# Optimization experiments

Hardware: AMD Instinct MI355X
Metric: run time of the kernel (lower is better)

## Reference

```python
import jax, jax.numpy as jnp
import numpy as np

N = 50000      # nodes
E = 500000     # edges
D = 128        # in_dim == out_dim
L = 4          # encoder_layers
G = 64         # graphs in batch
FIXED = 10000  # fixed_input_dim
BN_EPS = 1e-5


def setup_inputs() -> dict:
    key = jax.random.key(0)
    ks = jax.random.split(key, 14)
    s = 0.05
    feat_id = jax.random.randint(ks[0], (N,), 0, FIXED)
    edge_index = jax.random.randint(ks[1], (2, E), 0, N)
    # sorted graph assignment guaranteeing all G graphs are non-empty
    batch = (jnp.arange(N) * G) // N
    return {
        "feat_id": feat_id,
        "edge_index": edge_index,
        "batch": batch,
        # value_projection: Linear(FIXED, D); store weight.T as a lookup table
        "value_proj_w": jax.random.normal(ks[2], (FIXED, D)) * s,
        "value_proj_b": jax.random.normal(ks[3], (D,)) * s,
        "deg_emb": jax.random.normal(ks[4], (1001, D)) * s,
        # stacked per-layer GIN MLP params: Linear -> BN -> ReLU -> Linear
        "mlp_w1": jax.random.normal(ks[5], (L, D, D)) * s,
        "mlp_b1": jax.random.normal(ks[6], (L, D)) * s,
        "bn1_g": 1.0 + 0.1 * jax.random.normal(ks[7], (L, D)),
        "bn1_b": 0.1 * jax.random.normal(ks[8], (L, D)),
        "mlp_w2": jax.random.normal(ks[9], (L, D, D)) * s,
        "mlp_b2": jax.random.normal(ks[10], (L, D)) * s,
        # outer per-layer BatchNorm1d
        "bn2_g": 1.0 + 0.1 * jax.random.normal(ks[11], (L, D)),
        "bn2_b": 0.1 * jax.random.normal(ks[12], (L, D)),
    }


def _bn(x, g, b):
    # BatchNorm1d in training mode: batch stats over the node axis, biased var
    mu = jnp.mean(x, axis=0)
    var = jnp.mean(jnp.square(x - mu), axis=0)
    return g * (x - mu) * jax.lax.rsqrt(var + BN_EPS) + b


def reference(feat_id, edge_index, batch, value_proj_w, value_proj_b, deg_emb,
              mlp_w1, mlp_b1, bn1_g, bn1_b, mlp_w2, mlp_b2, bn2_g, bn2_b):
    src, dst = edge_index[0], edge_index[1]
    # one_hot(feat_id % FIXED) @ W.T + b  ==  gather of transposed weight rows
    h_attr = value_proj_w[feat_id % FIXED] + value_proj_b  # [N, D]
    # in-degree embedding (clamped to [0, 1000])
    in_deg = jax.ops.segment_sum(jnp.ones((E,), jnp.int32), dst, num_segments=N)
    h = h_attr + deg_emb[jnp.clip(in_deg, 0, 1000)]
    for i in range(L):
        # GIN: sum_{j in N(v)} h_j + (1 + eps) * h_v, eps = 0 (learn_eps=False)
        agg = jax.ops.segment_sum(h[src], dst, num_segments=N) + h
        z = jax.nn.relu(_bn(agg @ mlp_w1[i] + mlp_b1[i], bn1_g[i], bn1_b[i]))
        z = z @ mlp_w2[i] + mlp_b2[i]
        h = jax.nn.relu(_bn(z, bn2_g[i], bn2_b[i]))
    # global mean pool per graph
    gsum = jax.ops.segment_sum(h, batch, num_segments=G)       # [G, D]
    cnt = jax.ops.segment_sum(jnp.ones((N, 1)), batch, num_segments=G)
    graph_feature = gsum / jnp.maximum(cnt, 1.0)
    return graph_feature, h
```

## Files before the change

### kernel.cpp

```cpp
#include <hip/hip_runtime.h>

#define NN 50000
#define NE 500000
#define DD 128
#define NL 4
#define NG 64
#define FIXED_DIM 10000
#define BN_EPS 1e-5f
#define NB 196

typedef unsigned short u16;
typedef unsigned int u32;
typedef __attribute__((ext_vector_type(8))) short bf16x8;
typedef __attribute__((ext_vector_type(4))) float f32x4;

__device__ __forceinline__ float bf2f(u16 u) {
    return __uint_as_float(((u32)u) << 16);
}
__device__ __forceinline__ u16 f2bf(float f) {
    u32 u = __float_as_uint(f);
    return (u16)((u + 0x7FFFu + ((u >> 16) & 1u)) >> 16);
}
__device__ __forceinline__ float ldf(const void* p, size_t i, int isbf) {
    return isbf ? bf2f(((const u16*)p)[i]) : ((const float*)p)[i];
}

__global__ void k_pre(const void* __restrict__ vb, int* __restrict__ flag,
                      const int* __restrict__ batch, int* __restrict__ goff,
                      float* __restrict__ zbase, int zwords) {
    int b = blockIdx.x, t = threadIdx.x;
    if (b == 0) {
        __shared__ int ok[256];
        float v = (t < 128) ? bf2f(((const u16*)vb)[t]) : 0.f;
        ok[t] = (t < 128) ? ((fabsf(v) < 1000.f) ? 1 : 0) : 1;
        __syncthreads();
        for (int off = 128; off; off >>= 1) {
            if (t < off) ok[t] &= ok[t + off];
            __syncthreads();
        }
        if (t == 0) *flag = ok[0];
    } else if (b == 1) {
        if (t <= NG) {
            int lo = 0, hi = NN;
            while (lo < hi) {
                int mid = (lo + hi) >> 1;
                if (batch[mid] < t) lo = mid + 1; else hi = mid;
            }
            goff[t] = lo;
        }
    } else {
        int i = (b - 2) * 256 + t;
        if (i < zwords) zbase[i] = 0.f;
    }
}

__global__ void k_cvtswz(const void* b1, const void* b2, const void* g1,
                         const void* be1, const void* g2, const void* be2,
                         const void* __restrict__ w1, const void* __restrict__ w2,
                         float* __restrict__ pc, u16* __restrict__ Wsw,
                         const int* __restrict__ flag) {
    int b = blockIdx.x, tt = threadIdx.x;
    if (b < 12) {
        int t = b * 256 + tt;
        int p = t >> 9, j = t & 511;
        const void* s = (p == 0) ? b1 : (p == 1) ? b2 : (p == 2) ? g1
                      : (p == 3) ? be1 : (p == 4) ? g2 : be2;
        pc[t] = ldf(s, j, *flag);
    } else {
        int t = (b - 12) * 256 + tt;
        int m    = t >> 14;
        int idx  = t & 16383;
        int nt   = idx >> 11;
        int ks   = (idx >> 9) & 3;
        int lane = (idx >> 3) & 63;
        int j    = idx & 7;
        int row = ks * 32 + (lane >> 4) * 8 + j;
        int col = nt * 16 + (lane & 15);
        const void* src = (m < 4) ? w1 : w2;
        size_t off = (size_t)(m & 3) * DD * DD + (size_t)row * DD + col;
        Wsw[t] = f2bf(ldf(src, off, *flag));
    }
}

__global__ void k_deg(const int* __restrict__ dst, int* __restrict__ deg) {
    int i = blockIdx.x * 256 + threadIdx.x;
    if (i < NE) atomicAdd(&deg[dst[i]], 1);
}

__global__ void k_scan12(const int* __restrict__ deg, int* __restrict__ bsum,
                         int* __restrict__ sem) {
    __shared__ int S[256];
    __shared__ int lastB;
    int b = blockIdx.x, t = threadIdx.x;
    int i = b * 256 + t;
    S[t] = (i < NN) ? deg[i] : 0;
    __syncthreads();
    for (int off = 128; off; off >>= 1) {
        if (t < off) S[t] += S[t + off];
        __syncthreads();
    }
    if (t == 0) {
        atomicExch(&bsum[b], S[0]);
        __threadfence();
        lastB = (atomicAdd(&sem[0], 1) == gridDim.x - 1);
    }
    __syncthreads();
    if (!lastB) return;
    __threadfence();
    int v = (t < NB) ? atomicAdd(&bsum[t], 0) : 0;
    S[t] = v;
    __syncthreads();
    for (int off = 1; off < 256; off <<= 1) {
        int x = (t >= off) ? S[t - off] : 0;
        __syncthreads();
        S[t] += x;
        __syncthreads();
    }
    if (t < NB) bsum[t] = S[t] - v;
}

__global__ void k_scan3init(const int* __restrict__ deg, const int* __restrict__ bsum,
                            int* __restrict__ rowptr,
                            const int* __restrict__ feat, const void* __restrict__ vw,
                            const void* __restrict__ vb, const void* __restrict__ demb,
                            u16* __restrict__ B, const int* __restrict__ flag) {
    __shared__ int S[256];
    int b = blockIdx.x, t = threadIdx.x;
    if (b < NB) {
        int i = b * 256 + t;
        int v = (i < NN) ? deg[i] : 0;
        S[t] = v;
        __syncthreads();
        for (int off = 1; off < 256; off <<= 1) {
            int x = (t >= off) ? S[t - off] : 0;
            __syncthreads();
            S[t] += x;
            __syncthreads();
        }
        if (i < NN) rowptr[i] = bsum[b] + S[t] - v;
        if (i == NN - 1) rowptr[NN] = bsum[b] + S[t];
    } else {
        int idx = (b - NB) * 256 + t;
        if (idx >= NN * DD) return;
        int n = idx >> 7, c = idx & 127;
        int isbf = *flag;
        int f = feat[n] % FIXED_DIM;
        int dg = min(deg[n], 1000);
        B[idx] = f2bf(ldf(vw, (size_t)f * DD + c, isbf)
                    + ldf(vb, c, isbf)
                    + ldf(demb, (size_t)dg * DD + c, isbf));
    }
}

__global__ void k_fill(const int* __restrict__ src, const int* __restrict__ dst,
                       const int* __restrict__ rowptr, int* __restrict__ cursor,
                       int* __restrict__ colidx) {
    int e = blockIdx.x * 256 + threadIdx.x;
    if (e >= NE) return;
    int d = dst[e];
    int p = atomicAdd(&cursor[d], 1);
    colidx[rowptr[d] + p] = src[e];
}

template <bool AFF>
__global__ __launch_bounds__(256, 8) void k_aggr(
        const u16* __restrict__ B, const int* __restrict__ rowptr,
        const int* __restrict__ colidx,
        const float* __restrict__ gIn, const float* __restrict__ bIn,
        const float* __restrict__ sIn, const float* __restrict__ qIn,
        u16* __restrict__ Agg) {
    int n = blockIdx.x * 4 + (threadIdx.x >> 6);
    if (n >= NN) return;
    int c = (threadIdx.x & 63) * 2;
    float a0 = 1.f, b0 = 0.f, a1 = 1.f, b1 = 0.f;
    if (AFF) {
        float inv = 1.0f / (float)NN;
        float mu0 = sIn[c] * inv, mu1 = sIn[c + 1] * inv;
        float v0 = fmaxf(qIn[c] * inv - mu0 * mu0, 0.f);
        float v1 = fmaxf(qIn[c + 1] * inv - mu1 * mu1, 0.f);
        a0 = gIn[c] * rsqrtf(v0 + BN_EPS);
        a1 = gIn[c + 1] * rsqrtf(v1 + BN_EPS);
        b0 = bIn[c] - a0 * mu0;
        b1 = bIn[c + 1] - a1 * mu1;
    }
    u32 w = *(const u32*)&B[(size_t)n * DD + c];
    float x0 = bf2f((u16)(w & 0xFFFF)), x1 = bf2f((u16)(w >> 16));
    float s0 = AFF ? fmaxf(fmaf(a0, x0, b0), 0.f) : x0;
    float s1 = AFF ? fmaxf(fmaf(a1, x1, b1), 0.f) : x1;
    int lo = rowptr[n], hi = rowptr[n + 1];
    int j = lo;
    for (; j + 4 <= hi; j += 4) {
        int m0 = colidx[j], m1 = colidx[j + 1];
        int m2 = colidx[j + 2], m3 = colidx[j + 3];
        u32 w0 = *(const u32*)&B[(size_t)m0 * DD + c];
        u32 w1v = *(const u32*)&B[(size_t)m1 * DD + c];
        u32 w2v = *(const u32*)&B[(size_t)m2 * DD + c];
        u32 w3v = *(const u32*)&B[(size_t)m3 * DD + c];
        float y;
        y = bf2f((u16)(w0 & 0xFFFF)); s0 += AFF ? fmaxf(fmaf(a0, y, b0), 0.f) : y;
        y = bf2f((u16)(w0 >> 16));    s1 += AFF ? fmaxf(fmaf(a1, y, b1), 0.f) : y;
        y = bf2f((u16)(w1v & 0xFFFF)); s0 += AFF ? fmaxf(fmaf(a0, y, b0), 0.f) : y;
        y = bf2f((u16)(w1v >> 16));    s1 += AFF ? fmaxf(fmaf(a1, y, b1), 0.f) : y;
        y = bf2f((u16)(w2v & 0xFFFF)); s0 += AFF ? fmaxf(fmaf(a0, y, b0), 0.f) : y;
        y = bf2f((u16)(w2v >> 16));    s1 += AFF ? fmaxf(fmaf(a1, y, b1), 0.f) : y;
        y = bf2f((u16)(w3v & 0xFFFF)); s0 += AFF ? fmaxf(fmaf(a0, y, b0), 0.f) : y;
        y = bf2f((u16)(w3v >> 16));    s1 += AFF ? fmaxf(fmaf(a1, y, b1), 0.f) : y;
    }
    for (; j < hi; j++) {
        int m = colidx[j];
        w = *(const u32*)&B[(size_t)m * DD + c];
        x0 = bf2f((u16)(w & 0xFFFF)); x1 = bf2f((u16)(w >> 16));
        s0 += AFF ? fmaxf(fmaf(a0, x0, b0), 0.f) : x0;
        s1 += AFF ? fmaxf(fmaf(a1, x1, b1), 0.f) : x1;
    }
    *(u32*)&Agg[(size_t)n * DD + c] = ((u32)f2bf(s1) << 16) | (u32)f2bf(s0);
}

template <bool IN16, bool OUT16, bool AFF>
__global__ __launch_bounds__(256, 3) void k_gemm(
        const void* In, const u16* __restrict__ Wsw,
        const float* __restrict__ bias,
        const float* __restrict__ gIn, const float* __restrict__ bIn,
        const float* __restrict__ sIn, const float* __restrict__ qIn,
        void* Out, float* __restrict__ ssum, float* __restrict__ ssq,
        int nRows) {
    __shared__ u16 Wl[16384];
    __shared__ u16 At[64 * 136];
    __shared__ float affS[256];
    float* RedS = (float*)At;
    float* RedQ = RedS + 512;
    const int t = threadIdx.x;
    const int row0 = blockIdx.x * 64;

    if (AFF) {
        if (t < 128) {
            float inv = 1.0f / (float)NN;
            float mu = sIn[t] * inv;
            float var = fmaxf(qIn[t] * inv - mu * mu, 0.f);
            float a = gIn[t] * rsqrtf(var + BN_EPS);
            affS[t] = a;
            affS[128 + t] = bIn[t] - a * mu;
        }
        __syncthreads();
    }

    {
        const uint4* s = (const uint4*)Wsw;
        uint4* d = (uint4*)Wl;
        #pragma unroll
        for (int i = 0; i < 8; i++) d[t + i * 256] = s[t + i * 256];
    }
    if (IN16) {
        #pragma unroll
        for (int i = t; i < 1024; i += 256) {
            int r  = i >> 4;
            int c8 = (i & 15) * 8;
            int gr = row0 + r;
            uint4 v = make_uint4(0u, 0u, 0u, 0u);
            if (gr < nRows) v = *(const uint4*)&((const u16*)In)[(size_t)gr * DD + c8];
            *(uint4*)&At[r * 136 + c8] = v;
        }
    } else {
        #pragma unroll
        for (int i = t; i < 2048; i += 256) {
            int r  = i >> 5;
            int c4 = (i & 31) * 4;
            int gr = row0 + r;
            float4 v = make_float4(0.f, 0.f, 0.f, 0.f);
            if (gr < nRows) {
                v = *(const float4*)&((const float*)In)[(size_t)gr * DD + c4];
                if (AFF) {
                    v.x = fmaxf(fmaf(affS[c4 + 0], v.x, affS[128 + c4 + 0]), 0.f);
                    v.y = fmaxf(fmaf(affS[c4 + 1], v.y, affS[128 + c4 + 1]), 0.f);
                    v.z = fmaxf(fmaf(affS[c4 + 2], v.z, affS[128 + c4 + 2]), 0.f);
                    v.w = fmaxf(fmaf(affS[c4 + 3], v.w, affS[128 + c4 + 3]), 0.f);
                }
            }
            ushort4 o;
            o.x = f2bf(v.x); o.y = f2bf(v.y); o.z = f2bf(v.z); o.w = f2bf(v.w);
            *(ushort4*)&At[r * 136 + c4] = o;
        }
    }
    __syncthreads();

    const int w    = t >> 6;
    const int ln   = t & 63;
    const int quad = ln >> 4;
    const int lq   = ln & 15;

    f32x4 acc[8];
    #pragma unroll
    for (int nt = 0; nt < 8; nt++) acc[nt] = (f32x4){0.f, 0.f, 0.f, 0.f};

    const u16* aRow = &At[(w * 16 + lq) * 136 + quad * 8];
    #pragma unroll
    for (int ks = 0; ks < 4; ks++) {
        bf16x8 a = *(const bf16x8*)&aRow[ks * 32];
        #pragma unroll
        for (int nt = 0; nt < 8; nt++) {
            bf16x8 b = *(const bf16x8*)&Wl[((nt * 4 + ks) * 64 + ln) * 8];
            acc[nt] = __builtin_amdgcn_mfma_f32_16x16x32_bf16(a, b, acc[nt], 0, 0, 0);
        }
    }
    __syncthreads();

    const int rb = row0 + w * 16 + quad * 4;
    #pragma unroll
    for (int nt = 0; nt < 8; nt++) {
        int col = nt * 16 + lq;
        float bv = bias[col];
        float s = 0.f, q = 0.f;
        #pragma unroll
        for (int r = 0; r < 4; r++) {
            int gr = rb + r;
            if (gr < nRows) {
                float val = acc[nt][r] + bv;
                size_t o = (size_t)gr * DD + col;
                if (OUT16) ((u16*)Out)[o] = f2bf(val);
                else       ((float*)Out)[o] = val;
                s += val; q += val * val;
            }
        }
        s += __shfl_xor(s, 16); q += __shfl_xor(q, 16);
        s += __shfl_xor(s, 32); q += __shfl_xor(q, 32);
        if (quad == 0) { RedS[w * 128 + col] = s; RedQ[w * 128 + col] = q; }
    }
    __syncthreads();
    if (t < 128) {
        float s = RedS[t] + RedS[128 + t] + RedS[256 + t] + RedS[384 + t];
        float q = RedQ[t] + RedQ[128 + t] + RedQ[256 + t] + RedQ[384 + t];
        atomicAdd(&ssum[t], s);
        atomicAdd(&ssq[t], q);
    }
}

__global__ __launch_bounds__(256, 4) void k_upool(
        const u16* __restrict__ Bz,
        const float* __restrict__ gIn, const float* __restrict__ bIn,
        const float* __restrict__ sIn, const float* __restrict__ qIn,
        const int* __restrict__ batch, float* __restrict__ A,
        float* __restrict__ gsum, const int* __restrict__ goff,
        float* __restrict__ outw, int* __restrict__ sem) {
    const int t = threadIdx.x;
    const int c = t & 127;
    const int half = t >> 7;
    const int r0 = blockIdx.x * 64;
    float inv = 1.0f / (float)NN;
    float mu = sIn[c] * inv;
    float var = fmaxf(qIn[c] * inv - mu * mu, 0.f);
    float a = gIn[c] * rsqrtf(var + BN_EPS);
    float bb = bIn[c] - a * mu;
    float acc = 0.f;
    int curg = -1;
    for (int i = 0; i < 32; i++) {
        int r = r0 + half + 2 * i;
        if (r >= NN) break;
        int gg = batch[r];
        if (gg != curg) {
            if (curg >= 0) atomicAdd(&gsum[(size_t)curg * DD + c], acc);
            acc = 0.f; curg = gg;
        }
        float v = fmaxf(fmaf(a, bf2f(Bz[(size_t)r * DD + c]), bb), 0.f);
        A[(size_t)r * DD + c] = v;
        acc += v;
    }
    if (curg >= 0) atomicAdd(&gsum[(size_t)curg * DD + c], acc);

    __shared__ int lastF;
    if (t == 0) {
        __threadfence();
        lastF = (atomicAdd(&sem[1], 1) == gridDim.x - 1);
    }
    __syncthreads();
    if (!lastF) return;
    __threadfence();
    for (int i = t; i < NG * DD; i += 256) {
        int g = i >> 7;
        float cnt = fmaxf((float)(goff[g + 1] - goff[g]), 1.0f);
        outw[i] = atomicAdd(&gsum[i], 0.0f) / cnt;
    }
}

extern "C" void kernel_launch(void* const* d_in, const int* in_sizes, int n_in,
                              void* d_out, int out_size, void* d_ws, size_t ws_size,
                              hipStream_t stream) {
    const int* feat  = (const int*)d_in[0];
    const int* ei    = (const int*)d_in[1];
    const int* batch = (const int*)d_in[2];
    const void* vw   = d_in[3];
    const void* vb   = d_in[4];
    const void* demb = d_in[5];
    const void* w1   = d_in[6];
    const void* b1   = d_in[7];
    const void* g1   = d_in[8];
    const void* be1  = d_in[9];
    const void* w2   = d_in[10];
    const void* b2   = d_in[11];
    const void* g2   = d_in[12];
    const void* be2  = d_in[13];

    const int* src = ei;
    const int* dst = ei + NE;
    const size_t ND = (size_t)NN * DD;

    float* pc     = (float*)d_ws;
    int*   flag   = (int*)(pc + 3072);
    float* stats  = (float*)(flag + 64);
    float* gsum   = stats + 2048;
    int*   deg    = (int*)(gsum + 8192);
    int*   cursor = deg + NN;
    int*   sem    = cursor + NN;
    int*   bsum   = sem + 64;
    int*   goff   = bsum + 256;
    int*   rowptr = goff + 128;
    int*   colidx = rowptr + NN + 64;
    u16*   Wsw    = (u16*)(colidx + NE);
    u16*   B      = Wsw + 8 * 16384;
    u16*   Agg16  = B + ND;

    float* b1c  = pc;
    float* b2c  = pc + 512;
    float* g1c  = pc + 1024;
    float* be1c = pc + 1536;
    float* g2c  = pc + 2048;
    float* be2c = pc + 2560;
    float* sum1 = stats;
    float* sq1  = stats + 512;
    float* sum2 = stats + 1024;
    float* sq2  = stats + 1536;

    float* outw = (float*)d_out;
    float* A    = outw + (size_t)NG * DD;

    const int zwords = 2048 + 8192 + NN + NN + 64;
    const int gridND = (int)(ND / 256);
    const int gemmBlocks = (NN + 63) / 64;
    const int aggrBlocks = (NN + 3) / 4;

    k_pre<<<2 + (zwords + 255) / 256, 256, 0, stream>>>(vb, flag, batch, goff,
                                                        stats, zwords);
    k_cvtswz<<<12 + 512, 256, 0, stream>>>(b1, b2, g1, be1, g2, be2, w1, w2,
                                           pc, Wsw, flag);
    k_deg<<<(NE + 255) / 256, 256, 0, stream>>>(dst, deg);
    k_scan12<<<NB, 256, 0, stream>>>(deg, bsum, sem);
    k_scan3init<<<NB + gridND, 256, 0, stream>>>(deg, bsum, rowptr,
                                                 feat, vw, vb, demb, B, flag);
    k_fill<<<(NE + 255) / 256, 256, 0, stream>>>(src, dst, rowptr, cursor, colidx);

    for (int l = 0; l < NL; l++) {
        const u16* W1l = Wsw + (size_t)l * 16384;
        const u16* W2l = Wsw + (size_t)(4 + l) * 16384;
        if (l == 0) {
            k_aggr<false><<<aggrBlocks, 256, 0, stream>>>(
                B, rowptr, colidx, nullptr, nullptr, nullptr, nullptr, Agg16);
        } else {
            k_aggr<true><<<aggrBlocks, 256, 0, stream>>>(
                B, rowptr, colidx, g2c + (l - 1) * 128, be2c + (l - 1) * 128,
                sum2 + (l - 1) * 128, sq2 + (l - 1) * 128, Agg16);
        }
        k_gemm<true, false, false><<<gemmBlocks, 256, 0, stream>>>(
            Agg16, W1l, b1c + l * 128, nullptr, nullptr, nullptr, nullptr,
            A, sum1 + l * 128, sq1 + l * 128, NN);
        k_gemm<false, true, true><<<gemmBlocks, 256, 0, stream>>>(
            A, W2l, b2c + l * 128, g1c + l * 128, be1c + l * 128,
            sum1 + l * 128, sq1 + l * 128,
            B, sum2 + l * 128, sq2 + l * 128, NN);
    }
    k_upool<<<(NN + 63) / 64, 256, 0, stream>>>(
        B, g2c + 3 * 128, be2c + 3 * 128, sum2 + 3 * 128, sq2 + 3 * 128,
        batch, A, gsum, goff, outw, sem);
}
```

Measured before the change: 643.5 us.

## Double GEMM row tile to 128 and vectorize pooling kernel column access

The GEMM kernel now processes 128 rows per block, with each wave computing two 16-row MFMA tiles that share the same B fragments. This amortizes the per-block copy of the 32KB weight matrix into LDS across twice as many rows and halves the LDS reads of B per output. Occupancy drops to two blocks per CU because of the larger LDS and register footprint. Separately, the unpool/mean-pool kernel now has each thread handle two adjacent columns with 32-bit loads and float2 stores.

```diff
diff --git a/kernel.cpp b/kernel.cpp
--- a/kernel.cpp
+++ b/kernel.cpp
@@ -217,7 +217,7 @@
 }
 
 template <bool IN16, bool OUT16, bool AFF>
-__global__ __launch_bounds__(256, 3) void k_gemm(
+__global__ __launch_bounds__(256, 2) void k_gemm(
         const void* In, const u16* __restrict__ Wsw,
         const float* __restrict__ bias,
         const float* __restrict__ gIn, const float* __restrict__ bIn,
@@ -225,12 +225,12 @@
         void* Out, float* __restrict__ ssum, float* __restrict__ ssq,
         int nRows) {
     __shared__ u16 Wl[16384];
-    __shared__ u16 At[64 * 136];
+    __shared__ u16 At[128 * 136];
     __shared__ float affS[256];
     float* RedS = (float*)At;
     float* RedQ = RedS + 512;
     const int t = threadIdx.x;
-    const int row0 = blockIdx.x * 64;
+    const int row0 = blockIdx.x * 128;
 
     if (AFF) {
         if (t < 128) {
@@ -251,8 +251,7 @@
         for (int i = 0; i < 8; i++) d[t + i * 256] = s[t + i * 256];
     }
     if (IN16) {
-        #pragma unroll
-        for (int i = t; i < 1024; i += 256) {
+        for (int i = t; i < 2048; i += 256) {
             int r  = i >> 4;
             int c8 = (i & 15) * 8;
             int gr = row0 + r;
@@ -261,8 +260,7 @@
             *(uint4*)&At[r * 136 + c8] = v;
         }
     } else {
-        #pragma unroll
-        for (int i = t; i < 2048; i += 256) {
+        for (int i = t; i < 4096; i += 256) {
             int r  = i >> 5;
             int c4 = (i & 31) * 4;
             int gr = row0 + r;
@@ -288,23 +286,30 @@
     const int quad = ln >> 4;
     const int lq   = ln & 15;
 
-    f32x4 acc[8];
+    f32x4 acc0[8], acc1[8];
     #pragma unroll
-    for (int nt = 0; nt < 8; nt++) acc[nt] = (f32x4){0.f, 0.f, 0.f, 0.f};
-
-    const u16* aRow = &At[(w * 16 + lq) * 136 + quad * 8];
+    for (int nt = 0; nt < 8; nt++) {
+        acc0[nt] = (f32x4){0.f, 0.f, 0.f, 0.f};
+        acc1[nt] = (f32x4){0.f, 0.f, 0.f, 0.f};
+    }
+
+    const u16* aRow0 = &At[(w * 32 + lq) * 136 + quad * 8];
+    const u16* aRow1 = &At[(w * 32 + 16 + lq) * 136 + quad * 8];
     #pragma unroll
     for (int ks = 0; ks < 4; ks++) {
-        bf16x8 a = *(const bf16x8*)&aRow[ks * 32];
+        bf16x8 a0 = *(const bf16x8*)&aRow0[ks * 32];
+        bf16x8 a1 = *(const bf16x8*)&aRow1[ks * 32];
         #pragma unroll
         for (int nt = 0; nt < 8; nt++) {
             bf16x8 b = *(const bf16x8*)&Wl[((nt * 4 + ks) * 64 + ln) * 8];
-            acc[nt] = __builtin_amdgcn_mfma_f32_16x16x32_bf16(a, b, acc[nt], 0, 0, 0);
-        }
-    }
-    __syncthreads();
-
-    const int rb = row0 + w * 16 + quad * 4;
+            acc0[nt] = __builtin_amdgcn_mfma_f32_16x16x32_bf16(a0, b, acc0[nt], 0, 0, 0);
+            acc1[nt] = __builtin_amdgcn_mfma_f32_16x16x32_bf16(a1, b, acc1[nt], 0, 0, 0);
+        }
+    }
+    __syncthreads();
+
+    const int rb0 = row0 + w * 32 + quad * 4;
+    const int rb1 = rb0 + 16;
     #pragma unroll
     for (int nt = 0; nt < 8; nt++) {
         int col = nt * 16 + lq;
@@ -312,9 +317,20 @@
         float s = 0.f, q = 0.f;
         #pragma unroll
         for (int r = 0; r < 4; r++) {
-            int gr = rb + r;
+            int gr = rb0 + r;
             if (gr < nRows) {
-                float val = acc[nt][r] + bv;
+                float val = acc0[nt][r] + bv;
+                size_t o = (size_t)gr * DD + col;
+                if (OUT16) ((u16*)Out)[o] = f2bf(val);
+                else       ((float*)Out)[o] = val;
+                s += val; q += val * val;
+            }
+        }
+        #pragma unroll
+        for (int r = 0; r < 4; r++) {
+            int gr = rb1 + r;
+            if (gr < nRows) {
+                float val = acc1[nt][r] + bv;
                 size_t o = (size_t)gr * DD + col;
                 if (OUT16) ((u16*)Out)[o] = f2bf(val);
                 else       ((float*)Out)[o] = val;
@@ -342,29 +358,40 @@
         float* __restrict__ gsum, const int* __restrict__ goff,
         float* __restrict__ outw, int* __restrict__ sem) {
     const int t = threadIdx.x;
-    const int c = t & 127;
-    const int half = t >> 7;
+    const int c = (t & 63) * 2;
+    const int qv = t >> 6;
     const int r0 = blockIdx.x * 64;
     float inv = 1.0f / (float)NN;
-    float mu = sIn[c] * inv;
-    float var = fmaxf(qIn[c] * inv - mu * mu, 0.f);
-    float a = gIn[c] * rsqrtf(var + BN_EPS);
-    float bb = bIn[c] - a * mu;
-    float acc = 0.f;
+    float mu0 = sIn[c] * inv, mu1 = sIn[c + 1] * inv;
+    float v0 = fmaxf(qIn[c] * inv - mu0 * mu0, 0.f);
+    float v1 = fmaxf(qIn[c + 1] * inv - mu1 * mu1, 0.f);
+    float a0 = gIn[c] * rsqrtf(v0 + BN_EPS);
+    float a1 = gIn[c + 1] * rsqrtf(v1 + BN_EPS);
+    float b0 = bIn[c] - a0 * mu0;
+    float b1 = bIn[c + 1] - a1 * mu1;
+    float acc0 = 0.f, acc1 = 0.f;
     int curg = -1;
-    for (int i = 0; i < 32; i++) {
-        int r = r0 + half + 2 * i;
+    for (int i = 0; i < 16; i++) {
+        int r = r0 + qv + 4 * i;
         if (r >= NN) break;
         int gg = batch[r];
         if (gg != curg) {
-            if (curg >= 0) atomicAdd(&gsum[(size_t)curg * DD + c], acc);
-            acc = 0.f; curg = gg;
-        }
-        float v = fmaxf(fmaf(a, bf2f(Bz[(size_t)r * DD + c]), bb), 0.f);
-        A[(size_t)r * DD + c] = v;
-        acc += v;
-    }
-    if (curg >= 0) atomicAdd(&gsum[(size_t)curg * DD + c], acc);
+            if (curg >= 0) {
+                atomicAdd(&gsum[(size_t)curg * DD + c], acc0);
+                atomicAdd(&gsum[(size_t)curg * DD + c + 1], acc1);
+            }
+            acc0 = 0.f; acc1 = 0.f; curg = gg;
+        }
+        u32 wd = *(const u32*)&Bz[(size_t)r * DD + c];
+        float x0 = fmaxf(fmaf(a0, bf2f((u16)(wd & 0xFFFF)), b0), 0.f);
+        float x1 = fmaxf(fmaf(a1, bf2f((u16)(wd >> 16)), b1), 0.f);
+        *(float2*)&A[(size_t)r * DD + c] = make_float2(x0, x1);
+        acc0 += x0; acc1 += x1;
+    }
+    if (curg >= 0) {
+        atomicAdd(&gsum[(size_t)curg * DD + c], acc0);
+        atomicAdd(&gsum[(size_t)curg * DD + c + 1], acc1);
+    }
 
     __shared__ int lastF;
     if (t == 0) {
@@ -434,7 +461,7 @@
 
     const int zwords = 2048 + 8192 + NN + NN + 64;
     const int gridND = (int)(ND / 256);
-    const int gemmBlocks = (NN + 63) / 64;
+    const int gemmBlocks = (NN + 127) / 128;
     const int aggrBlocks = (NN + 3) / 4;
 
     k_pre<<<2 + (zwords + 255) / 256, 256, 0, stream>>>(vb, flag, batch, goff,
```

Result: faster. 557.5 us (-13.4%).
